# Kernel optimization log

Measured on AMD Instinct MI355X. Metric: run time of the kernel, lower is better.

## Reference

```python
import jax, jax.numpy as jnp
import numpy as np

B, SL, D, E, STEPS = 8, 1024, 128, 4, 5


def setup_inputs() -> dict:
    key = jax.random.key(0)
    ks = jax.random.split(key, 13)
    s = 0.02  # xavier-ish init scale
    return {
        "batchinput": jax.random.normal(ks[0], (B, SL, D), jnp.float32),
        # dense per-edge-type adjacency [B, sl, sl*E]; scaled so bmm output stays O(1)
        "batchgraphin": jax.random.uniform(ks[1], (B, SL, SL * E), jnp.float32) / SL,
        "batchgraphout": jax.random.uniform(ks[2], (B, SL, SL * E), jnp.float32) / SL,
        "W_in": jax.random.normal(ks[3], (E * D, E * D), jnp.float32) * s,
        "b_in": jnp.zeros((E * D,), jnp.float32),
        "W_out": jax.random.normal(ks[4], (E * D, E * D), jnp.float32) * s,
        "b_out": jnp.zeros((E * D,), jnp.float32),
        "W_r": jax.random.normal(ks[5], (D, 3 * D), jnp.float32) * s,
        "b_r": jnp.zeros((D,), jnp.float32),
        "W_z": jax.random.normal(ks[6], (D, 3 * D), jnp.float32) * s,
        "b_z": jnp.zeros((D,), jnp.float32),
        "W_t": jax.random.normal(ks[7], (D, 3 * D), jnp.float32) * s,
        "b_t": jnp.zeros((D,), jnp.float32),
    }


def reference(batchinput, batchgraphin, batchgraphout,
              W_in, b_in, W_out, b_out,
              W_r, b_r, W_z, b_z, W_t, b_t):
    out = batchinput  # [B, SL, D]
    for _ in range(STEPS):
        # tile node state across edge types: [B, SL, E*D]
        temp = jnp.broadcast_to(out[:, :, None, :], (B, SL, E, D)).reshape(B, SL, E * D)
        gi = (temp @ W_in.T + b_in).reshape(B, SL * E, D)
        gi = jnp.einsum('bse,bed->bsd', batchgraphin, gi)   # [B, SL, D]
        go = (temp @ W_out.T + b_out).reshape(B, SL * E, D)
        go = jnp.einsum('bse,bed->bsd', batchgraphout, go)  # [B, SL, D]
        # GRU-style gated update
        cat = jnp.concatenate([gi, go, out], axis=-1)       # [B, SL, 3D]
        r = jax.nn.sigmoid(cat @ W_r.T + b_r)
        z = jax.nn.sigmoid(cat @ W_z.T + b_z)
        h_hat = jnp.tanh(jnp.concatenate([gi, go, r * out], axis=-1) @ W_t.T + b_t)
        out = (1.0 - z) * out + z * h_hat
    return out
```

## Files before the change

kernel.cpp:

```cpp
#include <hip/hip_runtime.h>
#include <cstdint>
#include <cstddef>


typedef unsigned short u16;
typedef unsigned int u32;
typedef float f32x4 __attribute__((ext_vector_type(4)));
typedef short short8 __attribute__((ext_vector_type(8)));
typedef u16 u16x4 __attribute__((ext_vector_type(4)));
typedef u16 u16x8 __attribute__((ext_vector_type(8)));

__device__ __forceinline__ float b2f(u16 h) {
  union { u32 u; float f; } v; v.u = ((u32)h) << 16; return v.f;
}
__device__ __forceinline__ u16 f2bf(float f) {
  union { float f; u32 u; } v; v.f = f;
  u32 r = (v.u + 0x7fffu + ((v.u >> 16) & 1u)) >> 16;
  return (u16)r;
}
__device__ __forceinline__ float ldu(const void* p, size_t i, int flag) {
  return flag ? ((const float*)p)[i] : b2f(((const u16*)p)[i]);
}
__device__ __forceinline__ void gload_lds16(const void* g, void* l) {
  __builtin_amdgcn_global_load_lds((const __attribute__((address_space(1))) void*)g,
                                   (__attribute__((address_space(3))) void*)l,
                                   16, 0, 0);
}

__global__ void k_detect(const u16* g, int* flag) {
  __shared__ int bad;
  if (threadIdx.x == 0) bad = 0;
  __syncthreads();
  int any = 0;
  for (int i = threadIdx.x; i < 8192; i += 256) any |= (g[i] > 0x3B00);
  if (any) atomicOr(&bad, 1);
  __syncthreads();
  if (threadIdx.x == 0) *flag = bad;
}

__global__ void k_cvtf(const void* src, float* dst, int n, const int* flagp) {
  int i = blockIdx.x * 256 + threadIdx.x;
  if (i < n) dst[i] = ldu(src, i, *flagp);
}

__global__ void k_weff(const void* Win, const void* bin, const void* Wout, const void* bout,
                       u16* weffHT, u16* weffLT, float* biasf, const int* flagp) {
  int flag = *flagp;
  int idx = blockIdx.x * 256 + threadIdx.x;
  int j = idx >> 7, k = idx & 127;
  float s = 0.f;
  if (j < 512) {
#pragma unroll
    for (int e = 0; e < 4; e++) s += ldu(Win, (size_t)j * 512 + e * 128 + k, flag);
  } else {
#pragma unroll
    for (int e = 0; e < 4; e++) s += ldu(Wout, (size_t)(j - 512) * 512 + e * 128 + k, flag);
  }
  u16 h = f2bf(s);
  weffHT[(size_t)j * 128 + k] = h;
  weffLT[(size_t)j * 128 + k] = f2bf(s - b2f(h));
  if (idx < 1024) biasf[idx] = (idx < 512) ? ldu(bin, idx, flag) : ldu(bout, idx - 512, flag);
}

__global__ void k_wt(const void* W, const void* bv, float* WT, float* bf, const int* flagp) {
  int flag = *flagp;
  int idx = blockIdx.x * 256 + threadIdx.x;
  int n = idx / 384, k = idx % 384;
  WT[k * 128 + n] = ldu(W, idx, flag);
  if (idx < 128) bf[idx] = ldu(bv, idx, flag);
}

__global__ __launch_bounds__(512, 2) void kg_pre_mfma(
    const u16* __restrict__ weffHT, const u16* __restrict__ weffLT,
    const float* __restrict__ biasf, const float* __restrict__ outF,
    u16* __restrict__ gpreT) {
  __shared__ __align__(16) u16 AH[32 * 128];
  __shared__ __align__(16) u16 AL[32 * 128];
  __shared__ __align__(16) u16 ybuf[32 * 1024];
  int t = threadIdx.x;
  int b = blockIdx.y;
  int s0 = blockIdx.x * 32;
  {
    int row = t >> 4, c8 = (t & 15) * 8;
    const float* src = outF + (((size_t)(b * 1024 + s0 + row)) << 7) + c8;
    f32x4 x0 = *(const f32x4*)src;
    f32x4 x1 = *(const f32x4*)(src + 4);
    u16x8 vh, vl;
#pragma unroll
    for (int i = 0; i < 4; i++) {
      float x = x0[i]; u16 h = f2bf(x);
      vh[i] = h; vl[i] = f2bf(x - b2f(h));
      x = x1[i]; h = f2bf(x);
      vh[i + 4] = h; vl[i + 4] = f2bf(x - b2f(h));
    }
    int bc = (c8 * 2) ^ ((row & 7) << 4);
    *(u16x8*)((char*)AH + row * 256 + bc) = vh;
    *(u16x8*)((char*)AL + row * 256 + bc) = vl;
  }
  __syncthreads();
  int lane = t & 63, w = t >> 6;
  int wm = w >> 2, wn = w & 3;
  int lr = lane & 15, lk = lane >> 4;
  int n0 = wn * 256;
  int arow = wm * 16 + lr;
  int abase_row = arow * 256;
  int aswz = (arow & 7) << 4;
  f32x4 acc[16] = {};
#pragma unroll
  for (int kk = 0; kk < 4; kk++) {
    int kb = (kk * 64 + lk * 16) ^ aswz;
    short8 ah = *(const short8*)((const char*)AH + abase_row + kb);
    short8 al = *(const short8*)((const char*)AL + abase_row + kb);
    int wko = kk * 64 + lk * 16;
#pragma unroll
    for (int nf = 0; nf < 16; nf++) {
      int j = n0 + nf * 16 + lr;
      short8 wh = *(const short8*)((const char*)weffHT + (size_t)j * 256 + wko);
      short8 wl = *(const short8*)((const char*)weffLT + (size_t)j * 256 + wko);
      acc[nf] = __builtin_amdgcn_mfma_f32_16x16x32_bf16(ah, wh, acc[nf], 0, 0, 0);
      acc[nf] = __builtin_amdgcn_mfma_f32_16x16x32_bf16(ah, wl, acc[nf], 0, 0, 0);
      acc[nf] = __builtin_amdgcn_mfma_f32_16x16x32_bf16(al, wh, acc[nf], 0, 0, 0);
    }
  }
#pragma unroll
  for (int nf = 0; nf < 16; nf++) {
    int j = n0 + nf * 16 + lr;
    float bj = biasf[j];
#pragma unroll
    for (int i = 0; i < 4; i++) {
      int s = wm * 16 + lk * 4 + i;
      ybuf[s * 1024 + j] = f2bf(acc[nf][i] + bj);
    }
  }
  __syncthreads();
#pragma unroll
  for (int p = 0; p < 8; p++) {
    int row = p * 32 + (t >> 4);
    int gate = row >> 7, d = row & 127;
    int c = (t & 15) * 8;
    u16x8 v;
#pragma unroll
    for (int i = 0; i < 8; i++) {
      int k2 = c + i;
      v[i] = ybuf[(k2 >> 2) * 1024 + gate * 512 + (k2 & 3) * 128 + d];
    }
    *(u16x8*)(gpreT + (((size_t)((gate * 8 + b) * 128 + d)) << 12) + (size_t)s0 * 4 + c) = v;
  }
}

template <int WMODE>
__global__ __launch_bounds__(256, 2) void kg_bmm(
    const void* __restrict__ gin, const void* __restrict__ gout,
    u16* __restrict__ gB, int useGB, int writeStep,
    const u16* __restrict__ gpreT,
    float* __restrict__ P,
    const int* __restrict__ flagp) {
  __shared__ __align__(16) u16 bufA[2][4096];
  __shared__ __align__(16) u16 bufB[2][8192];

  int t = threadIdx.x;
  int lin0 = blockIdx.x + (blockIdx.y << 4) + (blockIdx.z << 8);
  int lin = ((lin0 & 7) << 6) + (lin0 >> 3);
  int mb = lin & 15, gb = (lin >> 4) & 15, kh = lin >> 8;
  int gate = gb >> 3, b = gb & 7;
  int ms0 = mb << 6;
  int kbase = kh << 11;

  int flag = *flagp;
  int doWrite = 0, srcBF = 1;
  const void* Asrc;
  size_t abase;
  if (WMODE == 0) {
    if (flag) { Asrc = gB;                abase = (((size_t)(gb * 1024 + ms0)) << 12) + kbase; }
    else      { Asrc = gate ? gout : gin; abase = (((size_t)(b  * 1024 + ms0)) << 12) + kbase; }
  } else {
    doWrite = useGB && flag && writeStep;
    srcBF = (flag == 0);
    Asrc = gate ? gout : gin;
    abase = (((size_t)(b * 1024 + ms0)) << 12) + kbase;
  }
  size_t gwbase = (((size_t)(gb * 1024 + ms0)) << 12) + kbase;

  int arow = t >> 4;
  int acolE = (t & 15) << 2;
  int acb = (t & 15) << 3;
  int aswz = (arow & 7) << 4;
  int lane = t & 63, w = t >> 6;
  int wm = w >> 1, wn = w & 1;
  int lr = lane & 15, lk = lane >> 4;
  int r0 = wm * 32 + lr;
  int c0 = wn * 64 + lr;
  int fswz = (lr & 7) << 4;

  f32x4 acc[2][4] = {};
  u16x4 ah[4];

  auto stageA_load = [&](int st) {
    size_t kk = abase + (size_t)st * 64;
    if (WMODE == 0 || srcBF) {
      const u16* p = (const u16*)Asrc;
#pragma unroll
      for (int it = 0; it < 4; it++)
        ah[it] = *(const u16x4*)(p + kk + (size_t)(arow + it * 16) * 4096 + acolE);
    } else {
      const float* p = (const float*)Asrc;
#pragma unroll
      for (int it = 0; it < 4; it++) {
        const f32x4* a = (const f32x4*)(p + kk + (size_t)(arow + it * 16) * 4096 + acolE);
        f32x4 af = doWrite ? __builtin_nontemporal_load(a) : *a;
        u16x4 v;
        v[0] = f2bf(af[0]); v[1] = f2bf(af[1]); v[2] = f2bf(af[2]); v[3] = f2bf(af[3]);
        ah[it] = v;
        if (doWrite)
          *(u16x4*)(gB + gwbase + (size_t)st * 64 + (size_t)(arow + it * 16) * 4096 + acolE) = v;
      }
    }
  };
  auto stageA_write = [&](int nb) {
#pragma unroll
    for (int it = 0; it < 4; it++)
      *(u16x4*)((char*)bufA[nb] + (arow + it * 16) * 128 + (acb ^ aswz)) = ah[it];
  };
  auto stageB = [&](int st, int nb) {
    size_t kk = (size_t)kbase + (size_t)st * 64;
#pragma unroll
    for (int c = 0; c < 4; c++) {
      int col = (w << 5) + (c << 3) + (lane >> 3);
      int j = (lane & 7) ^ (col & 7);
      const u16* g = gpreT + (((size_t)(gb * 128 + col)) << 12) + kk + (size_t)j * 8;
      u16* l = &bufB[nb][w * 2048 + c * 512];
      gload_lds16(g, l);
    }
  };
  auto compute = [&](int cur) {
    const char* A = (const char*)bufA[cur];
    const char* B = (const char*)bufB[cur];
#pragma unroll
    for (int ks = 0; ks < 2; ks++) {
      int kb = (ks * 64 + lk * 16) ^ fswz;
      short8 a0 = *(const short8*)(A + r0 * 128 + kb);
      short8 a1 = *(const short8*)(A + r0 * 128 + 2048 + kb);
#pragma unroll
      for (int nf = 0; nf < 4; nf++) {
        short8 bv = *(const short8*)(B + c0 * 128 + nf * 2048 + kb);
        acc[0][nf] = __builtin_amdgcn_mfma_f32_16x16x32_bf16(a0, bv, acc[0][nf], 0, 0, 0);
        acc[1][nf] = __builtin_amdgcn_mfma_f32_16x16x32_bf16(a1, bv, acc[1][nf], 0, 0, 0);
      }
    }
  };

  stageA_load(0);
  stageB(0, 0);
  stageA_write(0);
  __syncthreads();
  int cur = 0;
#pragma unroll 2
  for (int st = 0; st < 32; st++) {
    if (st < 31) { stageA_load(st + 1); stageB(st + 1, cur ^ 1); }
    compute(cur);
    if (st < 31) stageA_write(cur ^ 1);
    __syncthreads();
    cur ^= 1;
  }

  float* Pp = P + (((size_t)(kh * 16 + gb)) << 17);
#pragma unroll
  for (int mf = 0; mf < 2; mf++) {
#pragma unroll
    for (int nf = 0; nf < 4; nf++) {
      int rowb = ms0 + wm * 32 + mf * 16 + lk * 4;
      int col = wn * 64 + nf * 16 + lr;
#pragma unroll
      for (int j = 0; j < 4; j++)
        Pp[(size_t)(rowb + j) * 128 + col] = acc[mf][nf][j];
    }
  }
}

__global__ __launch_bounds__(256, 2) void kg_gate(
    const float* __restrict__ P, float* __restrict__ outF,
    const float* __restrict__ WTr, const float* __restrict__ WTz,
    const float* __restrict__ WTt,
    const float* __restrict__ brf, const float* __restrict__ bzf,
    const float* __restrict__ btf,
    const int* __restrict__ flagp, void* __restrict__ dout, int writeOut) {
  __shared__ __align__(16) float cs[16 * 384];
  __shared__ __align__(16) float rs[16 * 128];
  int t = threadIdx.x;
  int m0 = blockIdx.x * 16;
  int b = m0 >> 10;
  for (int i4 = t; i4 < 1536; i4 += 256) {
    int r = i4 / 96, q = i4 % 96;
    int m = m0 + r, s = m & 1023;
    f32x4 v;
    if (q < 64) {
      int gate = q >> 5;
      size_t idx = (((size_t)(gate * 8 + b)) << 17) + ((size_t)s << 7) + ((size_t)(q & 31) << 2);
      v = *(const f32x4*)(P + idx) + *(const f32x4*)(P + ((size_t)1 << 21) + idx);
    } else {
      v = *(const f32x4*)(outF + ((size_t)m << 7) + ((q - 64) << 2));
    }
    *(f32x4*)&cs[r * 384 + (q << 2)] = v;
  }
  __syncthreads();
  int n = t & 127, mh = t >> 7;
  float accR[8] = {}, accZ[8] = {}, accT[8] = {};
  for (int kq = 0; kq < 64; kq++) {
    float wr[4], wz[4], wt[4];
#pragma unroll
    for (int kl = 0; kl < 4; kl++) {
      wr[kl] = WTr[(kq * 4 + kl) * 128 + n];
      wz[kl] = WTz[(kq * 4 + kl) * 128 + n];
      wt[kl] = WTt[(kq * 4 + kl) * 128 + n];
    }
#pragma unroll
    for (int mi = 0; mi < 8; mi++) {
      f32x4 c = *(const f32x4*)&cs[(mh * 8 + mi) * 384 + kq * 4];
#pragma unroll
      for (int kl = 0; kl < 4; kl++) {
        accR[mi] += c[kl] * wr[kl];
        accZ[mi] += c[kl] * wz[kl];
        accT[mi] += c[kl] * wt[kl];
      }
    }
  }
  for (int kq = 64; kq < 96; kq++) {
    float wr[4], wz[4];
#pragma unroll
    for (int kl = 0; kl < 4; kl++) {
      wr[kl] = WTr[(kq * 4 + kl) * 128 + n];
      wz[kl] = WTz[(kq * 4 + kl) * 128 + n];
    }
#pragma unroll
    for (int mi = 0; mi < 8; mi++) {
      f32x4 c = *(const f32x4*)&cs[(mh * 8 + mi) * 384 + kq * 4];
#pragma unroll
      for (int kl = 0; kl < 4; kl++) {
        accR[mi] += c[kl] * wr[kl];
        accZ[mi] += c[kl] * wz[kl];
      }
    }
  }
  float bR = brf[n], bZ = bzf[n], bT = btf[n];
  float z8[8];
#pragma unroll
  for (int mi = 0; mi < 8; mi++) {
    int row = mh * 8 + mi;
    float r = 1.f / (1.f + __expf(-(accR[mi] + bR)));
    z8[mi] = 1.f / (1.f + __expf(-(accZ[mi] + bZ)));
    rs[row * 128 + n] = r * cs[row * 384 + 256 + n];
  }
  __syncthreads();
  for (int kq = 0; kq < 32; kq++) {
    float wt[4];
#pragma unroll
    for (int kl = 0; kl < 4; kl++) wt[kl] = WTt[(256 + kq * 4 + kl) * 128 + n];
#pragma unroll
    for (int mi = 0; mi < 8; mi++) {
      f32x4 c = *(const f32x4*)&rs[(mh * 8 + mi) * 128 + kq * 4];
#pragma unroll
      for (int kl = 0; kl < 4; kl++) accT[mi] += c[kl] * wt[kl];
    }
  }
  int flag = *flagp;
#pragma unroll
  for (int mi = 0; mi < 8; mi++) {
    int row = mh * 8 + mi;
    int m = m0 + row;
    size_t o = (size_t)m * 128 + n;
    float h = tanhf(accT[mi] + bT);
    float z = z8[mi];
    float ov = cs[row * 384 + 256 + n];
    float res = (1.f - z) * ov + z * h;
    outF[o] = res;
    if (writeOut) {
      if (flag) ((float*)dout)[o] = res;
      else      ((u16*)dout)[o] = f2bf(res);
    }
  }
}

extern "C" void kernel_launch(void* const* d_in, const int* in_sizes, int n_in,
                              void* d_out, int out_size, void* d_ws, size_t ws_size,
                              hipStream_t stream) {
  const void* X    = d_in[0];
  const void* Gin  = d_in[1];
  const void* Gout = d_in[2];
  const void* Win  = d_in[3];
  const void* bin  = d_in[4];
  const void* Wout = d_in[5];
  const void* bout = d_in[6];
  const void* Wr   = d_in[7];
  const void* br   = d_in[8];
  const void* Wz   = d_in[9];
  const void* bz   = d_in[10];
  const void* Wt   = d_in[11];
  const void* bt   = d_in[12];

  char* w = (char*)d_ws;
  auto alloc = [&](size_t n) { char* p = w; w += (n + 255) & ~(size_t)255; return p; };
  int*   flag    = (int*)alloc(4);
  u16*   weffHT  = (u16*)alloc((size_t)1024 * 128 * 2);
  u16*   weffLT  = (u16*)alloc((size_t)1024 * 128 * 2);
  float* biasf   = (float*)alloc(1024 * 4);
  float* WTr     = (float*)alloc((size_t)384 * 128 * 4);
  float* WTz     = (float*)alloc((size_t)384 * 128 * 4);
  float* WTt     = (float*)alloc((size_t)384 * 128 * 4);
  float* brf     = (float*)alloc(128 * 4);
  float* bzf     = (float*)alloc(128 * 4);
  float* btf     = (float*)alloc(128 * 4);
  float* outF    = (float*)alloc((size_t)8192 * 128 * 4);
  u16*   gpreT   = (u16*)alloc((size_t)16 * 128 * 4096 * 2);
  float* partial = (float*)alloc((size_t)2 * 16 * 1024 * 128 * 4);
  u16*   gB      = (u16*)alloc((size_t)2 * 8 * 1024 * 4096 * 2);
  int wsok = ((size_t)(w - (char*)d_ws) <= ws_size) ? 1 : 0;
  (void)in_sizes; (void)n_in; (void)out_size;

  k_detect<<<1, 256, 0, stream>>>((const u16*)Gin, flag);
  k_weff<<<512, 256, 0, stream>>>(Win, bin, Wout, bout, weffHT, weffLT, biasf, flag);
  k_wt<<<192, 256, 0, stream>>>(Wr, br, WTr, brf, flag);
  k_wt<<<192, 256, 0, stream>>>(Wz, bz, WTz, bzf, flag);
  k_wt<<<192, 256, 0, stream>>>(Wt, bt, WTt, btf, flag);
  k_cvtf<<<4096, 256, 0, stream>>>(X, outF, 1048576, flag);

  for (int step = 0; step < 5; step++) {
    kg_pre_mfma<<<dim3(32, 8), 512, 0, stream>>>(weffHT, weffLT, biasf, outF, gpreT);
    if (step == 0 || !wsok)
      kg_bmm<1><<<dim3(16, 16, 2), 256, 0, stream>>>(Gin, Gout, gB, wsok,
                                                     (step == 0) ? 1 : 0,
                                                     gpreT, partial, flag);
    else
      kg_bmm<0><<<dim3(16, 16, 2), 256, 0, stream>>>(Gin, Gout, gB, wsok, 0,
                                                     gpreT, partial, flag);
    kg_gate<<<512, 256, 0, stream>>>(partial, outF, WTr, WTz, WTt, brf, bzf, btf,
                                     flag, d_out, (step == 4) ? 1 : 0);
  }
}
```

Baseline: 1.057 ms.

## Move GRU gate matmuls to split-bf16 MFMA and defer bmm A-conversion

Rewrites the gate kernel to compute the r/z/t projections with bf16 MFMA instructions, using a hi/lo split (three MFMAs per tile) to keep near-fp32 accuracy instead of scalar fp32 FMAs. The weights are pre-split into bf16 hi/lo arrays by a single fused prep kernel. In the bmm kernel, the fp32-to-bf16 conversion and gB write of the A tile move from the load stage to the LDS-write stage, after compute, so global loads can stay in flight longer. Costs: more register pressure for the held fp32 values, and weights read straight from global memory in the MFMA loop.

Measured after the change: 892.4 us. 1.18x faster.

```diff
diff --git a/kernel.cpp b/kernel.cpp
--- a/kernel.cpp
+++ b/kernel.cpp
@@ -62,12 +62,22 @@
   if (idx < 1024) biasf[idx] = (idx < 512) ? ldu(bin, idx, flag) : ldu(bout, idx - 512, flag);
 }
 
-__global__ void k_wt(const void* W, const void* bv, float* WT, float* bf, const int* flagp) {
+__global__ void k_wt3(const void* Wr, const void* Wz, const void* Wt,
+                      const void* br, const void* bz, const void* bt,
+                      u16* wt3H, u16* wt3L,
+                      float* brf, float* bzf, float* btf, const int* flagp) {
   int flag = *flagp;
   int idx = blockIdx.x * 256 + threadIdx.x;
-  int n = idx / 384, k = idx % 384;
-  WT[k * 128 + n] = ldu(W, idx, flag);
-  if (idx < 128) bf[idx] = ldu(bv, idx, flag);
+  int g = idx / 49152, rem = idx % 49152;
+  const void* W = (g == 0) ? Wr : (g == 1) ? Wz : Wt;
+  float s = ldu(W, rem, flag);
+  u16 h = f2bf(s);
+  wt3H[(size_t)idx] = h;
+  wt3L[(size_t)idx] = f2bf(s - b2f(h));
+  if (rem < 128) {
+    float bv = ldu((g == 0) ? br : (g == 1) ? bz : bt, rem, flag);
+    ((g == 0) ? brf : (g == 1) ? bzf : btf)[rem] = bv;
+  }
 }
 
 __global__ __launch_bounds__(512, 2) void kg_pre_mfma(
@@ -193,7 +203,7 @@
   int fswz = (lr & 7) << 4;
 
   f32x4 acc[2][4] = {};
-  u16x4 ah[4];
+  f32x4 af[4]; u16x4 ah[4];
 
   auto stageA_load = [&](int st) {
     size_t kk = abase + (size_t)st * 64;
@@ -207,19 +217,22 @@
 #pragma unroll
       for (int it = 0; it < 4; it++) {
         const f32x4* a = (const f32x4*)(p + kk + (size_t)(arow + it * 16) * 4096 + acolE);
-        f32x4 af = doWrite ? __builtin_nontemporal_load(a) : *a;
-        u16x4 v;
-        v[0] = f2bf(af[0]); v[1] = f2bf(af[1]); v[2] = f2bf(af[2]); v[3] = f2bf(af[3]);
-        ah[it] = v;
-        if (doWrite)
-          *(u16x4*)(gB + gwbase + (size_t)st * 64 + (size_t)(arow + it * 16) * 4096 + acolE) = v;
+        af[it] = doWrite ? __builtin_nontemporal_load(a) : *a;
       }
     }
   };
-  auto stageA_write = [&](int nb) {
-#pragma unroll
-    for (int it = 0; it < 4; it++)
-      *(u16x4*)((char*)bufA[nb] + (arow + it * 16) * 128 + (acb ^ aswz)) = ah[it];
+  auto stageA_write = [&](int nb, int st) {
+#pragma unroll
+    for (int it = 0; it < 4; it++) {
+      int row = arow + it * 16;
+      u16x4 v;
+      if (WMODE == 0 || srcBF) v = ah[it];
+      else { v[0] = f2bf(af[it][0]); v[1] = f2bf(af[it][1]);
+             v[2] = f2bf(af[it][2]); v[3] = f2bf(af[it][3]); }
+      *(u16x4*)((char*)bufA[nb] + row * 128 + (acb ^ aswz)) = v;
+      if (WMODE == 1 && doWrite)
+        *(u16x4*)(gB + gwbase + (size_t)st * 64 + (size_t)row * 4096 + acolE) = v;
+    }
   };
   auto stageB = [&](int st, int nb) {
     size_t kk = (size_t)kbase + (size_t)st * 64;
@@ -251,14 +264,14 @@
 
   stageA_load(0);
   stageB(0, 0);
-  stageA_write(0);
+  stageA_write(0, 0);
   __syncthreads();
   int cur = 0;
 #pragma unroll 2
   for (int st = 0; st < 32; st++) {
     if (st < 31) { stageA_load(st + 1); stageB(st + 1, cur ^ 1); }
     compute(cur);
-    if (st < 31) stageA_write(cur ^ 1);
+    if (st < 31) stageA_write(cur ^ 1, st + 1);
     __syncthreads();
     cur ^= 1;
   }
@@ -277,15 +290,18 @@
   }
 }
 
-__global__ __launch_bounds__(256, 2) void kg_gate(
+__global__ __launch_bounds__(256, 2) void kg_gate_mfma(
     const float* __restrict__ P, float* __restrict__ outF,
-    const float* __restrict__ WTr, const float* __restrict__ WTz,
-    const float* __restrict__ WTt,
+    const u16* __restrict__ wt3H, const u16* __restrict__ wt3L,
     const float* __restrict__ brf, const float* __restrict__ bzf,
     const float* __restrict__ btf,
     const int* __restrict__ flagp, void* __restrict__ dout, int writeOut) {
-  __shared__ __align__(16) float cs[16 * 384];
-  __shared__ __align__(16) float rs[16 * 128];
+  __shared__ __align__(16) u16 csH[16 * 384];
+  __shared__ __align__(16) u16 csL[16 * 384];
+  __shared__ __align__(16) float outS[16 * 128];
+  __shared__ __align__(16) float zs[16 * 128];
+  __shared__ __align__(16) u16 rsH[16 * 128];
+  __shared__ __align__(16) u16 rsL[16 * 128];
   int t = threadIdx.x;
   int m0 = blockIdx.x * 16;
   int b = m0 >> 10;
@@ -299,83 +315,111 @@
       v = *(const f32x4*)(P + idx) + *(const f32x4*)(P + ((size_t)1 << 21) + idx);
     } else {
       v = *(const f32x4*)(outF + ((size_t)m << 7) + ((q - 64) << 2));
-    }
-    *(f32x4*)&cs[r * 384 + (q << 2)] = v;
-  }
-  __syncthreads();
-  int n = t & 127, mh = t >> 7;
-  float accR[8] = {}, accZ[8] = {}, accT[8] = {};
-  for (int kq = 0; kq < 64; kq++) {
-    float wr[4], wz[4], wt[4];
-#pragma unroll
-    for (int kl = 0; kl < 4; kl++) {
-      wr[kl] = WTr[(kq * 4 + kl) * 128 + n];
-      wz[kl] = WTz[(kq * 4 + kl) * 128 + n];
-      wt[kl] = WTt[(kq * 4 + kl) * 128 + n];
-    }
-#pragma unroll
-    for (int mi = 0; mi < 8; mi++) {
-      f32x4 c = *(const f32x4*)&cs[(mh * 8 + mi) * 384 + kq * 4];
-#pragma unroll
-      for (int kl = 0; kl < 4; kl++) {
-        accR[mi] += c[kl] * wr[kl];
-        accZ[mi] += c[kl] * wz[kl];
-        accT[mi] += c[kl] * wt[kl];
+      *(f32x4*)&outS[r * 128 + ((q - 64) << 2)] = v;
+    }
+    u16x4 vh, vl;
+#pragma unroll
+    for (int i = 0; i < 4; i++) {
+      u16 h = f2bf(v[i]);
+      vh[i] = h; vl[i] = f2bf(v[i] - b2f(h));
+    }
+    int byte = (q * 8) ^ ((r & 7) << 4);
+    *(u16x4*)((char*)csH + r * 768 + byte) = vh;
+    *(u16x4*)((char*)csL + r * 768 + byte) = vl;
+  }
+  __syncthreads();
+
+  int lane = t & 63, w = t >> 6;
+  int lr = lane & 15, lk = lane >> 4;
+  int aswz = (lr & 7) << 4;
+  const char* cH = (const char*)csH + lr * 768;
+  const char* cL = (const char*)csL + lr * 768;
+  f32x4 accR[2] = {}, accZ[2] = {}, accT[2] = {};
+  for (int kc = 0; kc < 12; kc++) {
+    int ab = (kc * 64 + lk * 16) ^ aswz;
+    short8 aH = *(const short8*)(cH + ab);
+    short8 aL = *(const short8*)(cL + ab);
+    int kb = kc * 64 + lk * 16;
+#pragma unroll
+    for (int nf = 0; nf < 2; nf++) {
+      int nl = w * 32 + nf * 16 + lr;
+      size_t offR = (size_t)nl * 768 + kb;
+      size_t offZ = (size_t)(128 + nl) * 768 + kb;
+      short8 bH = *(const short8*)((const char*)wt3H + offR);
+      short8 bL = *(const short8*)((const char*)wt3L + offR);
+      accR[nf] = __builtin_amdgcn_mfma_f32_16x16x32_bf16(aH, bH, accR[nf], 0, 0, 0);
+      accR[nf] = __builtin_amdgcn_mfma_f32_16x16x32_bf16(aH, bL, accR[nf], 0, 0, 0);
+      accR[nf] = __builtin_amdgcn_mfma_f32_16x16x32_bf16(aL, bH, accR[nf], 0, 0, 0);
+      bH = *(const short8*)((const char*)wt3H + offZ);
+      bL = *(const short8*)((const char*)wt3L + offZ);
+      accZ[nf] = __builtin_amdgcn_mfma_f32_16x16x32_bf16(aH, bH, accZ[nf], 0, 0, 0);
+      accZ[nf] = __builtin_amdgcn_mfma_f32_16x16x32_bf16(aH, bL, accZ[nf], 0, 0, 0);
+      accZ[nf] = __builtin_amdgcn_mfma_f32_16x16x32_bf16(aL, bH, accZ[nf], 0, 0, 0);
+      if (kc < 8) {
+        size_t offT = (size_t)(256 + nl) * 768 + kb;
+        bH = *(const short8*)((const char*)wt3H + offT);
+        bL = *(const short8*)((const char*)wt3L + offT);
+        accT[nf] = __builtin_amdgcn_mfma_f32_16x16x32_bf16(aH, bH, accT[nf], 0, 0, 0);
+        accT[nf] = __builtin_amdgcn_mfma_f32_16x16x32_bf16(aH, bL, accT[nf], 0, 0, 0);
+        accT[nf] = __builtin_amdgcn_mfma_f32_16x16x32_bf16(aL, bH, accT[nf], 0, 0, 0);
       }
     }
   }
-  for (int kq = 64; kq < 96; kq++) {
-    float wr[4], wz[4];
-#pragma unroll
-    for (int kl = 0; kl < 4; kl++) {
-      wr[kl] = WTr[(kq * 4 + kl) * 128 + n];
-      wz[kl] = WTz[(kq * 4 + kl) * 128 + n];
-    }
-#pragma unroll
-    for (int mi = 0; mi < 8; mi++) {
-      f32x4 c = *(const f32x4*)&cs[(mh * 8 + mi) * 384 + kq * 4];
-#pragma unroll
-      for (int kl = 0; kl < 4; kl++) {
-        accR[mi] += c[kl] * wr[kl];
-        accZ[mi] += c[kl] * wz[kl];
+#pragma unroll
+  for (int nf = 0; nf < 2; nf++) {
+    int nl = w * 32 + nf * 16 + lr;
+    float bR = brf[nl], bZ = bzf[nl];
+#pragma unroll
+    for (int i = 0; i < 4; i++) {
+      int row = lk * 4 + i;
+      float rv = 1.f / (1.f + __expf(-(accR[nf][i] + bR)));
+      float zv = 1.f / (1.f + __expf(-(accZ[nf][i] + bZ)));
+      zs[row * 128 + nl] = zv;
+      float rp = rv * outS[row * 128 + nl];
+      u16 h = f2bf(rp);
+      int byte = (nl * 2) ^ ((row & 7) << 4);
+      *(u16*)((char*)rsH + row * 256 + byte) = h;
+      *(u16*)((char*)rsL + row * 256 + byte) = f2bf(rp - b2f(h));
+    }
+  }
+  __syncthreads();
+  const char* rH = (const char*)rsH + lr * 256;
+  const char* rL = (const char*)rsL + lr * 256;
+#pragma unroll
+  for (int kc = 0; kc < 4; kc++) {
+    int ab = (kc * 64 + lk * 16) ^ aswz;
+    short8 aH = *(const short8*)(rH + ab);
+    short8 aL = *(const short8*)(rL + ab);
+    int kb = 512 + kc * 64 + lk * 16;
+#pragma unroll
+    for (int nf = 0; nf < 2; nf++) {
+      int nl = w * 32 + nf * 16 + lr;
+      size_t off = (size_t)(256 + nl) * 768 + kb;
+      short8 bH = *(const short8*)((const char*)wt3H + off);
+      short8 bL = *(const short8*)((const char*)wt3L + off);
+      accT[nf] = __builtin_amdgcn_mfma_f32_16x16x32_bf16(aH, bH, accT[nf], 0, 0, 0);
+      accT[nf] = __builtin_amdgcn_mfma_f32_16x16x32_bf16(aH, bL, accT[nf], 0, 0, 0);
+      accT[nf] = __builtin_amdgcn_mfma_f32_16x16x32_bf16(aL, bH, accT[nf], 0, 0, 0);
+    }
+  }
+  int flag = *flagp;
+#pragma unroll
+  for (int nf = 0; nf < 2; nf++) {
+    int nl = w * 32 + nf * 16 + lr;
+    float bT = btf[nl];
+#pragma unroll
+    for (int i = 0; i < 4; i++) {
+      int row = lk * 4 + i;
+      float h = tanhf(accT[nf][i] + bT);
+      float z = zs[row * 128 + nl];
+      float ov = outS[row * 128 + nl];
+      float res = (1.f - z) * ov + z * h;
+      size_t o = (size_t)(m0 + row) * 128 + nl;
+      outF[o] = res;
+      if (writeOut) {
+        if (flag) ((float*)dout)[o] = res;
+        else      ((u16*)dout)[o] = f2bf(res);
       }
-    }
-  }
-  float bR = brf[n], bZ = bzf[n], bT = btf[n];
-  float z8[8];
-#pragma unroll
-  for (int mi = 0; mi < 8; mi++) {
-    int row = mh * 8 + mi;
-    float r = 1.f / (1.f + __expf(-(accR[mi] + bR)));
-    z8[mi] = 1.f / (1.f + __expf(-(accZ[mi] + bZ)));
-    rs[row * 128 + n] = r * cs[row * 384 + 256 + n];
-  }
-  __syncthreads();
-  for (int kq = 0; kq < 32; kq++) {
-    float wt[4];
-#pragma unroll
-    for (int kl = 0; kl < 4; kl++) wt[kl] = WTt[(256 + kq * 4 + kl) * 128 + n];
-#pragma unroll
-    for (int mi = 0; mi < 8; mi++) {
-      f32x4 c = *(const f32x4*)&rs[(mh * 8 + mi) * 128 + kq * 4];
-#pragma unroll
-      for (int kl = 0; kl < 4; kl++) accT[mi] += c[kl] * wt[kl];
-    }
-  }
-  int flag = *flagp;
-#pragma unroll
-  for (int mi = 0; mi < 8; mi++) {
-    int row = mh * 8 + mi;
-    int m = m0 + row;
-    size_t o = (size_t)m * 128 + n;
-    float h = tanhf(accT[mi] + bT);
-    float z = z8[mi];
-    float ov = cs[row * 384 + 256 + n];
-    float res = (1.f - z) * ov + z * h;
-    outF[o] = res;
-    if (writeOut) {
-      if (flag) ((float*)dout)[o] = res;
-      else      ((u16*)dout)[o] = f2bf(res);
     }
   }
 }
@@ -403,9 +447,8 @@
   u16*   weffHT  = (u16*)alloc((size_t)1024 * 128 * 2);
   u16*   weffLT  = (u16*)alloc((size_t)1024 * 128 * 2);
   float* biasf   = (float*)alloc(1024 * 4);
-  float* WTr     = (float*)alloc((size_t)384 * 128 * 4);
-  float* WTz     = (float*)alloc((size_t)384 * 128 * 4);
-  float* WTt     = (float*)alloc((size_t)384 * 128 * 4);
+  u16*   wt3H    = (u16*)alloc((size_t)3 * 128 * 384 * 2);
+  u16*   wt3L    = (u16*)alloc((size_t)3 * 128 * 384 * 2);
   float* brf     = (float*)alloc(128 * 4);
   float* bzf     = (float*)alloc(128 * 4);
   float* btf     = (float*)alloc(128 * 4);
@@ -418,9 +461,7 @@
 
   k_detect<<<1, 256, 0, stream>>>((const u16*)Gin, flag);
   k_weff<<<512, 256, 0, stream>>>(Win, bin, Wout, bout, weffHT, weffLT, biasf, flag);
-  k_wt<<<192, 256, 0, stream>>>(Wr, br, WTr, brf, flag);
-  k_wt<<<192, 256, 0, stream>>>(Wz, bz, WTz, bzf, flag);
-  k_wt<<<192, 256, 0, stream>>>(Wt, bt, WTt, btf, flag);
+  k_wt3<<<576, 256, 0, stream>>>(Wr, Wz, Wt, br, bz, bt, wt3H, wt3L, brf, bzf, btf, flag);
   k_cvtf<<<4096, 256, 0, stream>>>(X, outF, 1048576, flag);
 
   for (int step = 0; step < 5; step++) {
@@ -432,7 +473,7 @@
     else
       kg_bmm<0><<<dim3(16, 16, 2), 256, 0, stream>>>(Gin, Gout, gB, wsok, 0,
                                                      gpreT, partial, flag);
-    kg_gate<<<512, 256, 0, stream>>>(partial, outF, WTr, WTz, WTt, brf, bzf, btf,
-                                     flag, d_out, (step == 4) ? 1 : 0);
-  }
-}
+    kg_gate_mfma<<<512, 256, 0, stream>>>(partial, outF, wt3H, wt3L, brf, bzf, btf,
+                                          flag, d_out, (step == 4) ? 1 : 0);
+  }
+}
```
